# Performance work log

Hardware: AMD Instinct MI355X
Metric: run time of the kernel (lower is better)

Reference implementation:

```python
import jax, jax.numpy as jnp
import numpy as np

D = 8192          # dimension (high_dim_mode since > 1000)
M = 1_600_000     # ~0.05 * D*(D-1) pairs after the i>j mask
RIEMANN_SHIFT = 0.5


def _lower_tri_pairs(rng, d, m):
    # Sample m unique strictly-lower-triangular (i, j) positions (i > j).
    total = d * (d - 1) // 2
    k = rng.choice(total, size=m, replace=False)
    kf = k.astype(np.float64)
    i = np.floor((1.0 + np.sqrt(1.0 + 8.0 * kf)) / 2.0).astype(np.int64)
    # fix possible off-by-one from float sqrt
    tri = i * (i - 1) // 2
    i = np.where(tri > k, i - 1, i)
    tri = i * (i - 1) // 2
    j = k - tri
    return i, j


def setup_inputs() -> dict:
    key = jax.random.key(0)
    k1, k2 = jax.random.split(key)
    rng = np.random.default_rng(0)

    i, j = _lower_tri_pairs(rng, D, M)
    interaction_indices = jnp.asarray(np.stack([i, j]))  # [2, M] int64

    local_scale = 1.0 / D ** 0.75
    h_local = jax.random.normal(k1, (D,), dtype=jnp.float32) * local_scale + RIEMANN_SHIFT

    dim_factor = 1.0 / (D ** 0.9 * np.log(D))
    V_interaction = jax.random.normal(k2, (M,), dtype=jnp.float32) * dim_factor

    return {
        "h_local": h_local,
        "V_interaction": V_interaction,
        "interaction_indices": interaction_indices,
        "dimension": D,
    }


def reference(h_local, V_interaction, interaction_indices, dimension) -> jnp.ndarray:
    d = h_local.shape[0]
    # scatter interaction values into strict lower triangle (set semantics,
    # indices are unique so set == torch assignment)
    H_int = jnp.zeros((d, d), dtype=h_local.dtype)
    H_int = H_int.at[interaction_indices[0], interaction_indices[1]].set(V_interaction)
    H_int = H_int + H_int.T  # symmetrize
    interaction_scale = 1.0 - 0.2 / np.sqrt(np.log(dimension))
    return jnp.diag(h_local) + H_int * interaction_scale
```

## Files before the change

kernel.cpp:

```cpp
#include <hip/hip_runtime.h>


typedef float f4 __attribute__((ext_vector_type(4)));

__global__ __launch_bounds__(256) void zero_fill_kernel(
    f4* __restrict__ out, long long n4)
{
    long long t = (long long)blockIdx.x * blockDim.x + threadIdx.x;
    if (t < n4) {
        f4 z = {0.f, 0.f, 0.f, 0.f};
        out[t] = z;
    }
}

__global__ __launch_bounds__(256) void scatter_kernel(
    float* __restrict__ out,
    const int* __restrict__ idx,
    const float* __restrict__ vals,
    const float* __restrict__ h_local,
    float scale,
    int m,
    int d,
    int logd)
{
    int k = blockIdx.x * blockDim.x + threadIdx.x;
    if (k >= m) return;
    int i = idx[k];
    int j = idx[m + k];
    float v = vals[k] * scale;
    out[((long long)i << logd) + j] = v;
    out[((long long)j << logd) + i] = v;
    if (k < d) {
        out[((long long)k << logd) + k] = h_local[k];
    }
}

extern "C" void kernel_launch(void* const* d_in, const int* in_sizes, int n_in,
                              void* d_out, int out_size, void* d_ws, size_t ws_size,
                              hipStream_t stream) {
    const float* h_local = (const float*)d_in[0];
    const float* V_int   = (const float*)d_in[1];
    const int*   idx     = (const int*)d_in[2];

    const int d = in_sizes[0];
    const int m = in_sizes[1];

    int logd = 0;
    while ((1 << logd) < d) ++logd;

    const double iscale_d = 1.0 - 0.2 / sqrt(log((double)d));
    const float  iscale   = (float)iscale_d;

    float* out = (float*)d_out;

    const long long n4 = ((long long)d * d) >> 2;
    const int block = 256;
    const long long grid_fill = (n4 + block - 1) / block;
    zero_fill_kernel<<<(dim3)(unsigned)grid_fill, block, 0, stream>>>((f4*)out, n4);

    const int grid_sc = (m + block - 1) / block;
    scatter_kernel<<<grid_sc, block, 0, stream>>>(out, idx, V_int, h_local,
                                                  iscale, m, d, logd);
}
```

Baseline: 364.2 us.

## Bin interactions per row and build dense rows in LDS

Replaces the full-matrix zero fill plus random scatter with three kernels. First, each interaction pair is binned into per-row buckets in workspace, using atomic counters for both (i,j) and (j,i). Then one block per row assembles that row in shared memory and streams it to global memory as coalesced vector stores. This removes the separate zero-fill pass and the scattered partial-line writes into the large output. In exchange it adds atomic contention on the row counters, extra workspace traffic, and the assumption that no row exceeds the bucket capacity, which is never checked. The new path only runs when d is 8192 and the workspace is large enough; otherwise it falls back to the old kernels.

```diff
diff --git a/kernel.cpp b/kernel.cpp
--- a/kernel.cpp
+++ b/kernel.cpp
@@ -2,6 +2,73 @@
 
 
 typedef float f4 __attribute__((ext_vector_type(4)));
+
+
+__global__ __launch_bounds__(256) void zero_counts_kernel(
+    unsigned int* __restrict__ counts, int d)
+{
+    int t = blockIdx.x * blockDim.x + threadIdx.x;
+    if (t < d) counts[t] = 0u;
+}
+
+__global__ __launch_bounds__(256) void bin_kernel(
+    const int* __restrict__ idx,
+    const float* __restrict__ vals,
+    unsigned int* __restrict__ counts,
+    uint2* __restrict__ buckets,
+    float scale,
+    int m,
+    int cap)
+{
+    int k = blockIdx.x * blockDim.x + threadIdx.x;
+    if (k >= m) return;
+    int i = idx[k];
+    int j = idx[m + k];
+    float v = vals[k] * scale;
+    unsigned int vb = __float_as_uint(v);
+    unsigned int p1 = atomicAdd(&counts[i], 1u);
+    buckets[(long long)i * cap + p1] = make_uint2((unsigned)j, vb);
+    unsigned int p2 = atomicAdd(&counts[j], 1u);
+    buckets[(long long)j * cap + p2] = make_uint2((unsigned)i, vb);
+}
+
+__global__ __launch_bounds__(256) void build_rows_kernel(
+    float* __restrict__ out,
+    const unsigned int* __restrict__ counts,
+    const uint2* __restrict__ buckets,
+    const float* __restrict__ h_local,
+    int d,
+    int logd,
+    int cap)
+{
+    __shared__ float row[8192];
+    const int r   = blockIdx.x;
+    const int tid = threadIdx.x;
+
+    f4* rowv = (f4*)row;
+    #pragma unroll
+    for (int it = 0; it < 8; ++it) {
+        f4 z = {0.f, 0.f, 0.f, 0.f};
+        rowv[it * 256 + tid] = z;
+    }
+    __syncthreads();
+
+    const unsigned int cnt = counts[r];
+    const uint2* b = buckets + (long long)r * cap;
+    for (unsigned int t = tid; t < cnt; t += 256) {
+        uint2 e = b[t];
+        row[e.x] = __uint_as_float(e.y);
+    }
+    if (tid == 0) row[r] = h_local[r];
+    __syncthreads();
+
+    f4* outv = (f4*)(out + ((long long)r << logd));
+    #pragma unroll
+    for (int it = 0; it < 8; ++it) {
+        outv[it * 256 + tid] = rowv[it * 256 + tid];
+    }
+}
+
 
 __global__ __launch_bounds__(256) void zero_fill_kernel(
     f4* __restrict__ out, long long n4)
@@ -18,10 +85,7 @@
     const int* __restrict__ idx,
     const float* __restrict__ vals,
     const float* __restrict__ h_local,
-    float scale,
-    int m,
-    int d,
-    int logd)
+    float scale, int m, int d, int logd)
 {
     int k = blockIdx.x * blockDim.x + threadIdx.x;
     if (k >= m) return;
@@ -30,9 +94,7 @@
     float v = vals[k] * scale;
     out[((long long)i << logd) + j] = v;
     out[((long long)j << logd) + i] = v;
-    if (k < d) {
-        out[((long long)k << logd) + k] = h_local[k];
-    }
+    if (k < d) out[((long long)k << logd) + k] = h_local[k];
 }
 
 extern "C" void kernel_launch(void* const* d_in, const int* in_sizes, int n_in,
@@ -52,13 +114,31 @@
     const float  iscale   = (float)iscale_d;
 
     float* out = (float*)d_out;
+    const int block = 256;
 
-    const long long n4 = ((long long)d * d) >> 2;
-    const int block = 256;
-    const long long grid_fill = (n4 + block - 1) / block;
-    zero_fill_kernel<<<(dim3)(unsigned)grid_fill, block, 0, stream>>>((f4*)out, n4);
+    const size_t counts_bytes = ((size_t)d * 4 + 4095) & ~(size_t)4095;
+    int cap = 0;
+    if (ws_size > counts_bytes) {
+        size_t avail = ws_size - counts_bytes;
+        size_t c = avail / ((size_t)d * 8);
+        cap = (int)(c > 1024 ? 1024 : c);
+    }
 
-    const int grid_sc = (m + block - 1) / block;
-    scatter_kernel<<<grid_sc, block, 0, stream>>>(out, idx, V_int, h_local,
-                                                  iscale, m, d, logd);
+    if (cap >= 512 && d == 8192) {
+        unsigned int* counts = (unsigned int*)d_ws;
+        uint2* buckets = (uint2*)((char*)d_ws + counts_bytes);
+
+        zero_counts_kernel<<<(d + block - 1) / block, block, 0, stream>>>(counts, d);
+        bin_kernel<<<(m + block - 1) / block, block, 0, stream>>>(
+            idx, V_int, counts, buckets, iscale, m, cap);
+        build_rows_kernel<<<d, block, 0, stream>>>(
+            out, counts, buckets, h_local, d, logd, cap);
+    } else {
+        const long long n4 = ((long long)d * d) >> 2;
+        const long long grid_fill = (n4 + block - 1) / block;
+        zero_fill_kernel<<<(dim3)(unsigned)grid_fill, block, 0, stream>>>((f4*)out, n4);
+        const int grid_sc = (m + block - 1) / block;
+        scatter_kernel<<<grid_sc, block, 0, stream>>>(out, idx, V_int, h_local,
+                                                      iscale, m, d, logd);
+    }
 }
```

Result: slower. 420.2 us (+15.4%).
